# Optimization experiments

Measured on AMD Instinct MI355X. Metric: run time of the kernel, lower is better.

Reference implementation:

```python
import jax, jax.numpy as jnp
import numpy as np

B, S, D, F, H, E = 2, 1024, 1024, 4096, 16, 8
EPS = 1e-5


def _layernorm(x, w, b):
    m = jnp.mean(x, -1, keepdims=True)
    v = jnp.var(x, -1, keepdims=True)
    return (x - m) * jax.lax.rsqrt(v + EPS) * w + b


def _rope(x):
    # rotary embedding applied over full embed dim (split-half convention)
    b, s, d = x.shape
    half = d // 2
    inv = 1.0 / (10000.0 ** (jnp.arange(half, dtype=jnp.float32) / half))
    ang = jnp.arange(s, dtype=jnp.float32)[:, None] * inv[None, :]  # [S, half]
    cos, sin = jnp.cos(ang), jnp.sin(ang)
    x1, x2 = x[..., :half], x[..., half:]
    return jnp.concatenate([x1 * cos - x2 * sin, x1 * sin + x2 * cos], -1)


def setup_inputs() -> dict:
    key = jax.random.key(0)
    ks = jax.random.split(key, 9)
    sc = 0.02
    return {
        "x": jax.random.normal(ks[0], (B, S, D), jnp.float32),
        "ln1_w": jnp.ones((D,), jnp.float32),
        "ln1_b": jnp.zeros((D,), jnp.float32),
        "ln2_w": jnp.ones((D,), jnp.float32),
        "ln2_b": jnp.zeros((D,), jnp.float32),
        "w_qkv": jax.random.normal(ks[1], (3 * D, D), jnp.float32) * sc,
        "b_qkv": jnp.zeros((3 * D,), jnp.float32),
        "w_out": jax.random.normal(ks[2], (D, D), jnp.float32) * sc,
        "b_out": jnp.zeros((D,), jnp.float32),
        "w_router": jax.random.normal(ks[3], (D, E), jnp.float32) * sc,
        "wi": jax.random.normal(ks[4], (E, D, F), jnp.float32) * sc,  # per-expert wi (no bias)
        "wo": jax.random.normal(ks[5], (E, F // 2, D), jnp.float32) * sc,  # swiglu halves ffn dim
    }


def reference(x, ln1_w, ln1_b, ln2_w, ln2_b, w_qkv, b_qkv, w_out, b_out, w_router, wi, wo):
    # ---- pre-norm self-attention block ----
    residual = x
    h = _layernorm(x, ln1_w, ln1_b)
    h = _rope(h)
    qkv = h @ w_qkv.T + b_qkv  # [B,S,3D]
    q, k, v = jnp.split(qkv, 3, axis=-1)
    hd = D // H
    to_heads = lambda t: t.reshape(B, S, H, hd).transpose(0, 2, 1, 3)
    q, k, v = to_heads(q), to_heads(k), to_heads(v)
    scale = 1.0 / np.sqrt(hd).astype(np.float32)
    att = jax.nn.softmax(jnp.einsum('bhqd,bhkd->bhqk', q, k) * scale, axis=-1)
    o = jnp.einsum('bhqk,bhkd->bhqd', att, v).transpose(0, 2, 1, 3).reshape(B, S, D)
    o = o @ w_out.T + b_out
    x = residual + o  # attn dropout is identity at eval

    # ---- pre-norm sparse MoE FFN block ----
    residual = x
    h = _layernorm(x, ln2_w, ln2_b)
    # top-1 router in float32
    logits = h.astype(jnp.float32) @ w_router  # [B,S,E]
    probs = jax.nn.softmax(logits, axis=-1)
    mask = jax.nn.one_hot(jnp.argmax(probs, -1), E, dtype=h.dtype)  # expert_mask
    gate = probs.astype(h.dtype) * mask  # router_probs * expert_mask, [B,S,E]
    # dense all-expert compute, masked combine (same math as gather/scatter loop)
    hid = jnp.einsum('bsd,edf->bsef', h, wi)  # [B,S,E,F]
    a, g = jnp.split(hid, 2, axis=-1)
    act = jax.nn.silu(a) * g  # SwiGLU, [B,S,E,F/2]
    y = jnp.einsum('bsef,efd,bse->bsd', act, wo, gate)
    x = residual + y
    return x, logits
```

## Files before the change

### kernel.cpp

```cpp
#include <hip/hip_runtime.h>
#include <hip/hip_bf16.h>
#include <math.h>

#define BB 2
#define SS 1024
#define DD 1024
#define FF 4096
#define HH 16
#define EE 8
#define MM (BB*SS)
#define MAX_TILES 24

typedef __attribute__((ext_vector_type(8))) short bf16x8;
typedef __attribute__((ext_vector_type(8))) short s16x8;
typedef __attribute__((ext_vector_type(4))) float f32x4;

#define OFF_WIT  ((size_t)0)
#define OFF_WOT  ((size_t)67108864)
#define OFF_WQH  ((size_t)100663296)
#define OFF_WQL  ((size_t)106954752)
#define OFF_WOH  ((size_t)113246208)
#define OFF_WOL  ((size_t)115343360)
#define OFF_H1H  ((size_t)117440512)
#define OFF_H1L  ((size_t)121634816)
#define OFF_QKV  ((size_t)125829120)
#define OFF_OH   ((size_t)150994944)
#define OFF_OL   ((size_t)155189248)
#define OFF_X2   ((size_t)159383552)
#define OFF_H2B  ((size_t)167772160)
#define OFF_ACT  ((size_t)171966464)
#define OFF_GATE ((size_t)180879360)
#define OFF_EID  ((size_t)180887552)
#define OFF_PERM ((size_t)180895744)
#define OFF_CNT  ((size_t)180903936)
#define OFF_FILL ((size_t)180903968)
#define OFF_NT   ((size_t)180904000)
#define OFF_TE   ((size_t)180904192)
#define OFF_TS   ((size_t)180904320)
#define OFF_TR   ((size_t)180904448)
#define OFF_KSH  OFF_WQH
#define OFF_KSL  (OFF_WQH + 4194304)
#define OFF_VTH  OFF_H1H
#define OFF_VTL  OFF_H1L

__device__ __forceinline__ void gload16(const void* g, void* l) {
    __builtin_amdgcn_global_load_lds(
        (const __attribute__((address_space(1))) unsigned int*)g,
        (__attribute__((address_space(3))) unsigned int*)l, 16, 0, 0);
}

__device__ __forceinline__ short bfh(float v) {
    __hip_bfloat16 h = __float2bfloat16(v);
    return *(short*)&h;
}
__device__ __forceinline__ float bf2f(short s) {
    __hip_bfloat16 h = *(__hip_bfloat16*)&s;
    return __bfloat162float(h);
}

__device__ __forceinline__ void split_write(float v, __hip_bfloat16* hp, __hip_bfloat16* lp, size_t idx) {
    __hip_bfloat16 h = __float2bfloat16(v);
    hp[idx] = h;
    lp[idx] = __float2bfloat16(v - __bfloat162float(h));
}

__device__ __forceinline__ void tcvt64_body(const float* __restrict__ in, __hip_bfloat16* __restrict__ out,
                                            int R, int C, int r0, int c0, float* tile ) {
    int t = threadIdx.x;
    {
        int ri = t >> 2, cj = (t & 3) * 16;
        const float* ip = &in[(size_t)(r0 + ri) * C + c0 + cj];
#pragma unroll
        for (int k = 0; k < 4; ++k) {
            float4 v = *(const float4*)(ip + k * 4);
            tile[ri * 65 + cj + k * 4 + 0] = v.x;
            tile[ri * 65 + cj + k * 4 + 1] = v.y;
            tile[ri * 65 + cj + k * 4 + 2] = v.z;
            tile[ri * 65 + cj + k * 4 + 3] = v.w;
        }
    }
    __syncthreads();
    {
        int co = t >> 2, rj = (t & 3) * 16;
        bf16x8 v8a, v8b;
#pragma unroll
        for (int q = 0; q < 8; ++q) v8a[q] = bfh(tile[(rj + q) * 65 + co]);
#pragma unroll
        for (int q = 0; q < 8; ++q) v8b[q] = bfh(tile[(rj + 8 + q) * 65 + co]);
        __hip_bfloat16* op = &out[(size_t)(c0 + co) * R + r0 + rj];
        *(bf16x8*)op = v8a;
        *(bf16x8*)(op + 8) = v8b;
    }
}

__global__ void k_phase0(const float* __restrict__ x, const float* __restrict__ ln1w,
                         const float* __restrict__ ln1b,
                         __hip_bfloat16* __restrict__ h1H, __hip_bfloat16* __restrict__ h1L,
                         const float* __restrict__ w_qkv, __hip_bfloat16* __restrict__ wqH,
                         __hip_bfloat16* __restrict__ wqL) {
    __shared__ __align__(16) float smem[1032];
    int bid = blockIdx.x, t = threadIdx.x;
    if (bid < 2048) {
        int m = bid, s = m & (SS - 1);
        float* row = smem;
        float* red = smem + 1024;
        const float* xp = x + (size_t)m * DD;
        float sum = 0.f, sumsq = 0.f;
#pragma unroll
        for (int l = 0; l < 4; ++l) {
            int i = t + l * 256;
            float v = xp[i];
            row[i] = v;
            sum += v; sumsq += v * v;
        }
#pragma unroll
        for (int off = 32; off; off >>= 1) {
            sum   += __shfl_xor(sum, off);
            sumsq += __shfl_xor(sumsq, off);
        }
        int wid = t >> 6, lane = t & 63;
        if (lane == 0) { red[wid] = sum; red[4 + wid] = sumsq; }
        __syncthreads();
        sum   = red[0] + red[1] + red[2] + red[3];
        sumsq = red[4] + red[5] + red[6] + red[7];
        float mean = sum * (1.f / DD);
        float var  = sumsq * (1.f / DD) - mean * mean;
        float rstd = rsqrtf(var + 1e-5f);
        size_t base = (size_t)m * DD;
        const float kln = logf(10000.f) / 512.f;
#pragma unroll
        for (int l = 0; l < 2; ++l) {
            int i = t + l * 256;
            float n1 = (row[i]       - mean) * rstd * ln1w[i]       + ln1b[i];
            float n2 = (row[i + 512] - mean) * rstd * ln1w[i + 512] + ln1b[i + 512];
            float inv = expf(-(float)i * kln);
            float ang = (float)s * inv;
            float c = cosf(ang), sn = sinf(ang);
            split_write(n1 * c - n2 * sn,  h1H, h1L, base + i);
            split_write(n1 * sn + n2 * c, h1H, h1L, base + i + 512);
        }
    } else {
        int idx = (bid - 2048) * 256 + t;
        float4 v = ((const float4*)w_qkv)[idx];
        split_write(v.x, wqH, wqL, (size_t)idx * 4 + 0);
        split_write(v.y, wqH, wqL, (size_t)idx * 4 + 1);
        split_write(v.z, wqH, wqL, (size_t)idx * 4 + 2);
        split_write(v.w, wqH, wqL, (size_t)idx * 4 + 3);
    }
}

__global__ void k_qkv_mega(const __hip_bfloat16* __restrict__ Ah, const __hip_bfloat16* __restrict__ Al,
                           const __hip_bfloat16* __restrict__ Bh, const __hip_bfloat16* __restrict__ Bl,
                           const float* __restrict__ bias, float* __restrict__ Cf,
                           const float* __restrict__ wi, __hip_bfloat16* __restrict__ wiT,
                           const float* __restrict__ wo, __hip_bfloat16* __restrict__ woT,
                           const float* __restrict__ w_out, __hip_bfloat16* __restrict__ woH,
                           __hip_bfloat16* __restrict__ woL) {
    __shared__ __align__(16) char smem[32768];
    int bid = blockIdx.x;
    const int t = threadIdx.x;
    if (bid < 384) {
        const int N = 3072, K = DD;
        short* AsH = (short*)smem;
        short* AsL = (short*)(smem + 8192);
        short* BsH = (short*)(smem + 16384);
        short* BsL = (short*)(smem + 24576);
        int n0 = (bid % 24) * 128, m0 = (bid / 24) * 128;
        const int w = t >> 6, lane = t & 63;
        const int wr = w >> 1, wc = w & 1;
        const int sid = w * 64 + lane;

        f32x4 acc[4][4] = {};

        for (int k0 = 0; k0 < K; k0 += 32) {
#pragma unroll
            for (int j = 0; j < 2; ++j) {
                int id = j * 256 + sid;
                int rrow = id >> 2, sl = id & 3;
                int slog = sl ^ ((rrow >> 1) & 3);
                size_t lbase = (size_t)(j * 256 + w * 64) * 8;
                size_t gaoff = (size_t)(m0 + rrow) * K + k0 + slog * 8;
                gload16(Ah + gaoff, &AsH[lbase]);
                gload16(Al + gaoff, &AsL[lbase]);
                size_t gboff = (size_t)(n0 + rrow) * K + k0 + slog * 8;
                gload16(Bh + gboff, &BsH[lbase]);
                gload16(Bl + gboff, &BsL[lbase]);
            }
            __syncthreads();
            bf16x8 ah[4], al[4], bh[4], bl[4];
#pragma unroll
            for (int i = 0; i < 4; ++i) {
                int ra = wr * 64 + i * 16 + (lane & 15);
                int pa = (lane >> 4) ^ ((ra >> 1) & 3);
                ah[i] = *(const bf16x8*)&AsH[ra * 32 + pa * 8];
                al[i] = *(const bf16x8*)&AsL[ra * 32 + pa * 8];
                int rb = wc * 64 + i * 16 + (lane & 15);
                int pb = (lane >> 4) ^ ((rb >> 1) & 3);
                bh[i] = *(const bf16x8*)&BsH[rb * 32 + pb * 8];
                bl[i] = *(const bf16x8*)&BsL[rb * 32 + pb * 8];
            }
#pragma unroll
            for (int i = 0; i < 4; ++i)
#pragma unroll
                for (int n = 0; n < 4; ++n) {
                    acc[i][n] = __builtin_amdgcn_mfma_f32_16x16x32_bf16(ah[i], bh[n], acc[i][n], 0, 0, 0);
                    acc[i][n] = __builtin_amdgcn_mfma_f32_16x16x32_bf16(ah[i], bl[n], acc[i][n], 0, 0, 0);
                    acc[i][n] = __builtin_amdgcn_mfma_f32_16x16x32_bf16(al[i], bh[n], acc[i][n], 0, 0, 0);
                }
            __syncthreads();
        }

        int cn = n0 + wc * 64 + (lane & 15);
#pragma unroll
        for (int i = 0; i < 4; ++i) {
#pragma unroll
            for (int n = 0; n < 4; ++n) {
                int col = cn + n * 16;
#pragma unroll
                for (int q = 0; q < 4; ++q) {
                    int r = wr * 64 + i * 16 + (lane >> 4) * 4 + q;
                    Cf[(size_t)(m0 + r) * N + col] = acc[i][n][q] + bias[col];
                }
            }
        }
    } else if (bid < 8576) {
        int j = bid - 384;
        int e = j >> 10, rem = j & 1023;
        int ry = rem >> 6, cx = rem & 63;
        tcvt64_body(wi + (size_t)e * DD * FF, wiT + (size_t)e * DD * FF,
                    1024, 4096, ry * 64, cx * 64, (float*)smem);
    } else if (bid < 12672) {
        int j = bid - 8576;
        int e = j >> 9, rem = j & 511;
        int ry = rem >> 4, cx = rem & 15;
        tcvt64_body(wo + (size_t)e * 2048 * 1024, woT + (size_t)e * 2048 * 1024,
                    2048, 1024, ry * 64, cx * 64, (float*)smem);
    } else {
        int idx = (bid - 12672) * 256 + t;
        float4 v = ((const float4*)w_out)[idx];
        split_write(v.x, woH, woL, (size_t)idx * 4 + 0);
        split_write(v.y, woH, woL, (size_t)idx * 4 + 1);
        split_write(v.z, woH, woL, (size_t)idx * 4 + 2);
        split_write(v.w, woH, woL, (size_t)idx * 4 + 3);
    }
}

__global__ void k_mfma_split1(const __hip_bfloat16* __restrict__ Ah, const __hip_bfloat16* __restrict__ Al,
                              const __hip_bfloat16* __restrict__ Bh, const __hip_bfloat16* __restrict__ Bl,
                              const float* __restrict__ bias, const float* __restrict__ addsrc,
                              float* __restrict__ Cf, int M, int N, int K, int* __restrict__ zero17) {
    __shared__ __align__(16) short AsH[128 * 32];
    __shared__ __align__(16) short AsL[128 * 32];
    __shared__ __align__(16) short BsH[128 * 32];
    __shared__ __align__(16) short BsL[128 * 32];
    int m0 = blockIdx.y * 128, n0 = blockIdx.x * 128;
    const int t = threadIdx.x;
    if (blockIdx.x == 0 && blockIdx.y == 0 && t < 17) zero17[t] = 0;
    const int w = t >> 6, lane = t & 63;
    const int wr = w >> 1, wc = w & 1;
    const int sid = w * 64 + lane;

    f32x4 acc[4][4] = {};

    for (int k0 = 0; k0 < K; k0 += 32) {
#pragma unroll
        for (int j = 0; j < 2; ++j) {
            int id = j * 256 + sid;
            int rrow = id >> 2, sl = id & 3;
            int slog = sl ^ ((rrow >> 1) & 3);
            size_t lbase = (size_t)(j * 256 + w * 64) * 8;
            size_t gaoff = (size_t)(m0 + rrow) * K + k0 + slog * 8;
            gload16(Ah + gaoff, &AsH[lbase]);
            gload16(Al + gaoff, &AsL[lbase]);
            size_t gboff = (size_t)(n0 + rrow) * K + k0 + slog * 8;
            gload16(Bh + gboff, &BsH[lbase]);
            gload16(Bl + gboff, &BsL[lbase]);
        }
        __syncthreads();
        bf16x8 ah[4], al[4], bh[4], bl[4];
#pragma unroll
        for (int i = 0; i < 4; ++i) {
            int ra = wr * 64 + i * 16 + (lane & 15);
            int pa = (lane >> 4) ^ ((ra >> 1) & 3);
            ah[i] = *(const bf16x8*)&AsH[ra * 32 + pa * 8];
            al[i] = *(const bf16x8*)&AsL[ra * 32 + pa * 8];
            int rb = wc * 64 + i * 16 + (lane & 15);
            int pb = (lane >> 4) ^ ((rb >> 1) & 3);
            bh[i] = *(const bf16x8*)&BsH[rb * 32 + pb * 8];
            bl[i] = *(const bf16x8*)&BsL[rb * 32 + pb * 8];
        }
#pragma unroll
        for (int i = 0; i < 4; ++i)
#pragma unroll
            for (int n = 0; n < 4; ++n) {
                acc[i][n] = __builtin_amdgcn_mfma_f32_16x16x32_bf16(ah[i], bh[n], acc[i][n], 0, 0, 0);
                acc[i][n] = __builtin_amdgcn_mfma_f32_16x16x32_bf16(ah[i], bl[n], acc[i][n], 0, 0, 0);
                acc[i][n] = __builtin_amdgcn_mfma_f32_16x16x32_bf16(al[i], bh[n], acc[i][n], 0, 0, 0);
            }
        __syncthreads();
    }

    int cn = n0 + wc * 64 + (lane & 15);
#pragma unroll
    for (int i = 0; i < 4; ++i) {
#pragma unroll
        for (int n = 0; n < 4; ++n) {
            int col = cn + n * 16;
#pragma unroll
            for (int q = 0; q < 4; ++q) {
                int r = wr * 64 + i * 16 + (lane >> 4) * 4 + q;
                Cf[(size_t)(m0 + r) * N + col] =
                    acc[i][n][q] + bias[col] + addsrc[(size_t)(m0 + r) * N + col];
            }
        }
    }
}

__global__ void k_moe_up(const __hip_bfloat16* __restrict__ A,
                         const __hip_bfloat16* __restrict__ Bt,
                         __hip_bfloat16* __restrict__ act,
                         const int* __restrict__ perm,
                         const int* __restrict__ te, const int* __restrict__ ts,
                         const int* __restrict__ tr, const int* __restrict__ ntl) {
    __shared__ __align__(16) short As[128 * 32];
    __shared__ __align__(16) short Bs[128 * 32];
    __shared__ int permS[128];
    int tile = blockIdx.y;
    if (tile >= *ntl) return;
    int e = te[tile], rs = ts[tile], rows = tr[tile];
    if (threadIdx.x < 128) {
        int r = threadIdx.x;
        permS[r] = (r < rows) ? perm[rs + r] : 0;
    }
    __syncthreads();
    int c0 = blockIdx.x * 64;
    const int t = threadIdx.x;
    const int w = t >> 6, lane = t & 63;
    const int wr = w >> 1, wc = w & 1;
    const int sid = w * 64 + lane;
    const int g = lane >> 4, r16 = lane & 15;

    const __hip_bfloat16* Bp = Bt + (size_t)e * FF * DD;

    f32x4 acc[4][4] = {};

    for (int k0 = 0; k0 < DD; k0 += 32) {
#pragma unroll
        for (int j = 0; j < 2; ++j) {
            int id = j * 256 + sid;
            int rrow = id >> 2, sl = id & 3;
            int slog = sl ^ ((rrow >> 1) & 3);
            size_t lbase = (size_t)(j * 256 + w * 64) * 8;
            gload16(A + (size_t)permS[rrow] * DD + k0 + slog * 8, &As[lbase]);
            int q = rrow >> 4, rr = rrow & 15;
            int wrow = c0 + (q >> 2) * 32 + ((q & 3) >> 1) * 16 + rr + (q & 1) * 2048;
            gload16(Bp + (size_t)wrow * DD + k0 + slog * 8, &Bs[lbase]);
        }
        __syncthreads();
        bf16x8 af[4], bfr[4];
#pragma unroll
        for (int i = 0; i < 4; ++i) {
            int ra = wr * 64 + i * 16 + r16;
            int pa = g ^ ((ra >> 1) & 3);
            af[i] = *(const bf16x8*)&As[ra * 32 + pa * 8];
            int rb = wc * 64 + i * 16 + r16;
            int pb = g ^ ((rb >> 1) & 3);
            bfr[i] = *(const bf16x8*)&Bs[rb * 32 + pb * 8];
        }
#pragma unroll
        for (int i = 0; i < 4; ++i)
#pragma unroll
            for (int n = 0; n < 4; ++n)
                acc[i][n] = __builtin_amdgcn_mfma_f32_16x16x32_bf16(af[i], bfr[n], acc[i][n], 0, 0, 0);
        __syncthreads();
    }

#pragma unroll
    for (int i = 0; i < 4; ++i) {
#pragma unroll
        for (int p2 = 0; p2 < 2; ++p2) {
            int col = c0 + wc * 32 + p2 * 16 + r16;
#pragma unroll
            for (int q = 0; q < 4; ++q) {
                int r = wr * 64 + i * 16 + g * 4 + q;
                if (r < rows) {
                    float a  = acc[i][2 * p2][q];
                    float gv = acc[i][2 * p2 + 1][q];
                    act[(size_t)(rs + r) * 2048 + col] =
                        __float2bfloat16((a / (1.f + expf(-a))) * gv);
                }
            }
        }
    }
}

__global__ void k_moe_dn(const __hip_bfloat16* __restrict__ A,
                         const __hip_bfloat16* __restrict__ Bt,
                         const float* __restrict__ addsrc, float* __restrict__ Cf,
                         const int* __restrict__ perm,
                         const int* __restrict__ te, const int* __restrict__ ts,
                         const int* __restrict__ tr, const int* __restrict__ ntl,
                         const float* __restrict__ gate) {
    __shared__ __align__(16) short As[128 * 32];
    __shared__ __align__(16) short Bs[128 * 32];
    __shared__ int permS[128];
    int tile = blockIdx.y;
    if (tile >= *ntl) return;
    int e = te[tile], rs = ts[tile], rows = tr[tile];
    if (threadIdx.x < 128) {
        int r = threadIdx.x;
        permS[r] = (r < rows) ? perm[rs + r] : 0;
    }
    __syncthreads();
    int n0 = blockIdx.x * 128;
    const int t = threadIdx.x;
    const int w = t >> 6, lane = t & 63;
    const int wr = w >> 1, wc = w & 1;
    const int sid = w * 64 + lane;
    const int K = FF / 2;

    const __hip_bfloat16* Bp = Bt + (size_t)e * DD * (FF / 2);

    f32x4 acc[4][4] = {};

    for (int k0 = 0; k0 < K; k0 += 32) {
#pragma unroll
        for (int j = 0; j < 2; ++j) {
            int id = j * 256 + sid;
            int rrow = id >> 2, sl = id & 3;
            int slog = sl ^ ((rrow >> 1) & 3);
            size_t lbase = (size_t)(j * 256 + w * 64) * 8;
            gload16(A + (size_t)(rs + rrow) * K + k0 + slog * 8, &As[lbase]);
            gload16(Bp + (size_t)(n0 + rrow) * K + k0 + slog * 8, &Bs[lbase]);
        }
        __syncthreads();
        bf16x8 af[4], bfr[4];
#pragma unroll
        for (int i = 0; i < 4; ++i) {
            int ra = wr * 64 + i * 16 + (lane & 15);
            int pa = (lane >> 4) ^ ((ra >> 1) & 3);
            af[i] = *(const bf16x8*)&As[ra * 32 + pa * 8];
            int rb = wc * 64 + i * 16 + (lane & 15);
            int pb = (lane >> 4) ^ ((rb >> 1) & 3);
            bfr[i] = *(const bf16x8*)&Bs[rb * 32 + pb * 8];
        }
#pragma unroll
        for (int i = 0; i < 4; ++i)
#pragma unroll
            for (int n = 0; n < 4; ++n)
                acc[i][n] = __builtin_amdgcn_mfma_f32_16x16x32_bf16(af[i], bfr[n], acc[i][n], 0, 0, 0);
        __syncthreads();
    }

    int cn = n0 + wc * 64 + (lane & 15);
#pragma unroll
    for (int i = 0; i < 4; ++i) {
#pragma unroll
        for (int n = 0; n < 4; ++n) {
            int col = cn + n * 16;
#pragma unroll
            for (int q = 0; q < 4; ++q) {
                int r = wr * 64 + i * 16 + (lane >> 4) * 4 + q;
                if (r >= rows) continue;
                int tok = permS[r];
                Cf[(size_t)tok * DD + col] = addsrc[(size_t)tok * DD + col] + gate[tok] * acc[i][n][q];
            }
        }
    }
}

__global__ void k_prep(const float* __restrict__ qkv, short* __restrict__ KH, short* __restrict__ KL,
                       short* __restrict__ VH, short* __restrict__ VL) {
    __shared__ float tile[64][65];
    int b = blockIdx.z, h = blockIdx.y, s0 = blockIdx.x * 64;
    int t = threadIdx.x;
    int row = t >> 2, c0 = (t & 3) * 16;
    const float* kp = qkv + (size_t)(b * SS + s0 + row) * 3072 + 1024 + h * 64 + c0;
    const float* vp = kp + 1024;
    {
        size_t krow = ((size_t)(b * HH + h) * SS + s0 + row) * 64;
        int key = (s0 + row) & 7;
#pragma unroll
        for (int g2 = 0; g2 < 2; ++g2) {
            s16x8 hv, lv;
#pragma unroll
            for (int j = 0; j < 8; ++j) {
                float v = kp[g2 * 8 + j];
                short hh = bfh(v);
                hv[j] = hh; lv[j] = bfh(v - bf2f(hh));
            }
            int p = ((c0 >> 3) + g2) ^ key;
            *(s16x8*)&KH[krow + p * 8] = hv;
            *(s16x8*)&KL[krow + p * 8] = lv;
        }
    }
#pragma unroll
    for (int j = 0; j < 16; ++j) tile[row][c0 + j] = vp[j];
    __syncthreads();
    {
        int d = t >> 2, sc = (t & 3) * 16;
        size_t vrow = ((size_t)(b * HH + h) * 64 + d) * SS + s0;
        int key = d & 7;
#pragma unroll
        for (int g2 = 0; g2 < 2; ++g2) {
            s16x8 hv, lv;
#pragma unroll
            for (int j = 0; j < 8; ++j) {
                float v = tile[sc + g2 * 8 + j][d];
                short hh = bfh(v);
                hv[j] = hh; lv[j] = bfh(v - bf2f(hh));
            }
            int p = ((sc >> 3) + g2) ^ key;
            *(s16x8*)&VH[vrow + p * 8] = hv;
            *(s16x8*)&VL[vrow + p * 8] = lv;
        }
    }
}

#define LDP 72
__global__ __launch_bounds__(512, 1)
void k_attn_mfma(const float* __restrict__ qkv,
                 const short* __restrict__ KH, const short* __restrict__ KL,
                 const short* __restrict__ VH, const short* __restrict__ VL,
                 __hip_bfloat16* __restrict__ ohi, __hip_bfloat16* __restrict__ olo) {
    __shared__ __align__(16) short Ks[2][64 * 64], Kl2[2][64 * 64], Vs[2][64 * 64], Vl2[2][64 * 64];
    __shared__ __align__(16) short PhS[8][16 * LDP], PlS[8][16 * LDP];
    int id = blockIdx.x;
    int xcd = id & 7, slot = id >> 3;
    int bh = xcd * 4 + (slot >> 3);
    int q0 = (slot & 7) * 128;
    int b = bh >> 4, h = bh & 15;
    int t = threadIdx.x;
    int w = t >> 6, lane = t & 63;
    int g = lane >> 4, r16 = lane & 15;
    int srow = t >> 3, sslot = t & 7;

    const size_t kbase = ((size_t)bh * SS) * 64;
    const size_t vbase = ((size_t)bh * 64) * SS;

    bf16x8 qfh[2], qfl[2];
    {
        const float* qp = qkv + (size_t)(b * SS + q0 + w * 16 + r16) * 3072 + h * 64;
#pragma unroll
        for (int ks = 0; ks < 2; ++ks) {
            float vv[8];
            *(float4*)&vv[0] = *(const float4*)(qp + ks * 32 + g * 8);
            *(float4*)&vv[4] = *(const float4*)(qp + ks * 32 + g * 8 + 4);
#pragma unroll
            for (int j = 0; j < 8; ++j) {
                float sv = vv[j] * 0.125f;
                short hh = bfh(sv);
                qfh[ks][j] = hh;
                qfl[ks][j] = bfh(sv - bf2f(hh));
            }
        }
    }

    float mrun[4], lrun[4];
    f32x4 oacc[4] = {};
#pragma unroll
    for (int q = 0; q < 4; ++q) { mrun[q] = -1e30f; lrun[q] = 0.f; }

    gload16(KH + kbase + (size_t)srow * 64 + sslot * 8, &Ks[0][w * 512]);
    gload16(KL + kbase + (size_t)srow * 64 + sslot * 8, &Kl2[0][w * 512]);
    gload16(VH + vbase + (size_t)srow * SS + sslot * 8, &Vs[0][w * 512]);
    gload16(VL + vbase + (size_t)srow * SS + sslot * 8, &Vl2[0][w * 512]);
    __syncthreads();

    int cur = 0;
    for (int k0 = 0; k0 < SS; k0 += 64) {
        if (k0 + 64 < SS) {
            int kn = k0 + 64;
            gload16(KH + kbase + (size_t)(kn + srow) * 64 + sslot * 8, &Ks[cur ^ 1][w * 512]);
            gload16(KL + kbase + (size_t)(kn + srow) * 64 + sslot * 8, &Kl2[cur ^ 1][w * 512]);
            gload16(VH + vbase + (size_t)srow * SS + kn + sslot * 8,   &Vs[cur ^ 1][w * 512]);
            gload16(VL + vbase + (size_t)srow * SS + kn + sslot * 8,   &Vl2[cur ^ 1][w * 512]);
        }

        f32x4 accs[4] = {};
#pragma unroll
        for (int ks = 0; ks < 2; ++ks) {
            bf16x8 kfh[4], kfl[4];
#pragma unroll
            for (int n = 0; n < 4; ++n) {
                int rb = n * 16 + r16;
                int p = (ks * 4 + g) ^ (r16 & 7);
                kfh[n] = *(const bf16x8*)&Ks[cur][rb * 64 + p * 8];
                kfl[n] = *(const bf16x8*)&Kl2[cur][rb * 64 + p * 8];
            }
            __builtin_amdgcn_s_setprio(1);
#pragma unroll
            for (int n = 0; n < 4; ++n) {
                accs[n] = __builtin_amdgcn_mfma_f32_16x16x32_bf16(qfh[ks], kfh[n], accs[n], 0, 0, 0);
                accs[n] = __builtin_amdgcn_mfma_f32_16x16x32_bf16(qfh[ks], kfl[n], accs[n], 0, 0, 0);
                accs[n] = __builtin_amdgcn_mfma_f32_16x16x32_bf16(qfl[ks], kfh[n], accs[n], 0, 0, 0);
            }
            __builtin_amdgcn_s_setprio(0);
        }

        float mn[4], corr[4], psum[4];
#pragma unroll
        for (int q = 0; q < 4; ++q) {
            float m = fmaxf(fmaxf(accs[0][q], accs[1][q]), fmaxf(accs[2][q], accs[3][q]));
            m = fmaxf(m, __shfl_xor(m, 1));
            m = fmaxf(m, __shfl_xor(m, 2));
            m = fmaxf(m, __shfl_xor(m, 4));
            m = fmaxf(m, __shfl_xor(m, 8));
            mn[q] = fmaxf(mrun[q], m);
            corr[q] = expf(mrun[q] - mn[q]);
            mrun[q] = mn[q];
            psum[q] = 0.f;
        }
#pragma unroll
        for (int n = 0; n < 4; ++n)
#pragma unroll
            for (int q = 0; q < 4; ++q) {
                float p = expf(accs[n][q] - mn[q]);
                psum[q] += p;
                short ph = bfh(p);
                PhS[w][(g * 4 + q) * LDP + n * 16 + r16] = ph;
                PlS[w][(g * 4 + q) * LDP + n * 16 + r16] = bfh(p - bf2f(ph));
            }
#pragma unroll
        for (int q = 0; q < 4; ++q) {
            psum[q] += __shfl_xor(psum[q], 1);
            psum[q] += __shfl_xor(psum[q], 2);
            psum[q] += __shfl_xor(psum[q], 4);
            psum[q] += __shfl_xor(psum[q], 8);
            lrun[q] = lrun[q] * corr[q] + psum[q];
#pragma unroll
            for (int n = 0; n < 4; ++n) oacc[n][q] *= corr[q];
        }

#pragma unroll
        for (int ks = 0; ks < 2; ++ks) {
            bf16x8 vfh[4], vfl[4];
#pragma unroll
            for (int n = 0; n < 4; ++n) {
                int rb = n * 16 + r16;
                int p = (ks * 4 + g) ^ (r16 & 7);
                vfh[n] = *(const bf16x8*)&Vs[cur][rb * 64 + p * 8];
                vfl[n] = *(const bf16x8*)&Vl2[cur][rb * 64 + p * 8];
            }
            bf16x8 pfh = *(const bf16x8*)&PhS[w][r16 * LDP + ks * 32 + g * 8];
            bf16x8 pfl = *(const bf16x8*)&PlS[w][r16 * LDP + ks * 32 + g * 8];
            __builtin_amdgcn_s_setprio(1);
#pragma unroll
            for (int n = 0; n < 4; ++n) {
                oacc[n] = __builtin_amdgcn_mfma_f32_16x16x32_bf16(pfh, vfh[n], oacc[n], 0, 0, 0);
                oacc[n] = __builtin_amdgcn_mfma_f32_16x16x32_bf16(pfh, vfl[n], oacc[n], 0, 0, 0);
                oacc[n] = __builtin_amdgcn_mfma_f32_16x16x32_bf16(pfl, vfh[n], oacc[n], 0, 0, 0);
            }
            __builtin_amdgcn_s_setprio(0);
        }
        __syncthreads();
        cur ^= 1;
    }

    float invl[4];
#pragma unroll
    for (int q = 0; q < 4; ++q) invl[q] = 1.f / lrun[q];
#pragma unroll
    for (int n = 0; n < 4; ++n) {
        int col = h * 64 + n * 16 + r16;
#pragma unroll
        for (int q = 0; q < 4; ++q) {
            int rowg = b * SS + q0 + w * 16 + g * 4 + q;
            split_write(oacc[n][q] * invl[q], ohi, olo, (size_t)rowg * DD + col);
        }
    }
}

__global__ void k_ln2_router(const float* __restrict__ x2, const float* __restrict__ w,
                             const float* __restrict__ b, const float* __restrict__ wr,
                             __hip_bfloat16* __restrict__ h2b, float* __restrict__ logits,
                             float* __restrict__ gate, int* __restrict__ eid,
                             int* __restrict__ counts) {
    int m = blockIdx.x, t = threadIdx.x;
    __shared__ float red[8];
    __shared__ float racc[4][8];
    const float* xp = x2 + (size_t)m * DD;
    float v[4];
    float sum = 0.f, sumsq = 0.f;
#pragma unroll
    for (int l = 0; l < 4; ++l) {
        v[l] = xp[t + l * 256];
        sum += v[l]; sumsq += v[l] * v[l];
    }
#pragma unroll
    for (int off = 32; off; off >>= 1) {
        sum   += __shfl_xor(sum, off);
        sumsq += __shfl_xor(sumsq, off);
    }
    int wid = t >> 6, lane = t & 63;
    if (lane == 0) { red[wid] = sum; red[4 + wid] = sumsq; }
    __syncthreads();
    sum   = red[0] + red[1] + red[2] + red[3];
    sumsq = red[4] + red[5] + red[6] + red[7];
    float mean = sum * (1.f / DD);
    float var  = sumsq * (1.f / DD) - mean * mean;
    float rstd = rsqrtf(var + 1e-5f);
    float acc[EE] = {};
#pragma unroll
    for (int l = 0; l < 4; ++l) {
        int i = t + l * 256;
        float hv = (v[l] - mean) * rstd * w[i] + b[i];
        h2b[(size_t)m * DD + i] = __float2bfloat16(hv);
        const float* wp = wr + (size_t)i * EE;
#pragma unroll
        for (int n = 0; n < EE; ++n) acc[n] += hv * wp[n];
    }
#pragma unroll
    for (int off = 32; off; off >>= 1)
#pragma unroll
        for (int n = 0; n < EE; ++n) acc[n] += __shfl_xor(acc[n], off);
    if (lane == 0)
#pragma unroll
        for (int n = 0; n < EE; ++n) racc[wid][n] = acc[n];
    __syncthreads();
    if (t == 0) {
        float lg[EE];
#pragma unroll
        for (int n = 0; n < EE; ++n) lg[n] = racc[0][n] + racc[1][n] + racc[2][n] + racc[3][n];
        float mx = lg[0]; int best = 0;
#pragma unroll
        for (int n = 1; n < EE; ++n) if (lg[n] > mx) { mx = lg[n]; best = n; }
        float den = 0.f;
#pragma unroll
        for (int n = 0; n < EE; ++n) den += expf(lg[n] - mx);
        gate[m] = 1.f / den;
        eid[m] = best;
        atomicAdd(&counts[best], 1);
#pragma unroll
        for (int n = 0; n < EE; ++n) logits[(size_t)m * EE + n] = lg[n];
    }
}

__global__ void k_offscatter(const int* __restrict__ counts,
                             int* __restrict__ te, int* __restrict__ ts, int* __restrict__ tr,
                             int* __restrict__ ntl, const int* __restrict__ eid,
                             int* __restrict__ fill, int* __restrict__ perm) {
    __shared__ int soffs[EE];
    int t = threadIdx.x;
    if (t == 0) {
        int off = 0, nt = 0;
        for (int e = 0; e < EE; ++e) {
            soffs[e] = off;
            int c = counts[e];
            for (int t0 = 0; t0 < c; t0 += 128) {
                te[nt] = e; ts[nt] = off + t0; tr[nt] = (c - t0 < 128) ? (c - t0) : 128; ++nt;
            }
            off += c;
        }
        *ntl = nt;
    }
    __syncthreads();
#pragma unroll
    for (int tok = t; tok < MM; tok += 1024) {
        int e = eid[tok];
        int pos = soffs[e] + atomicAdd(&fill[e], 1);
        perm[pos] = tok;
    }
}

extern "C" void kernel_launch(void* const* d_in, const int* in_sizes, int n_in,
                              void* d_out, int out_size, void* d_ws, size_t ws_size,
                              hipStream_t stream) {
    const float* x     = (const float*)d_in[0];
    const float* ln1w  = (const float*)d_in[1];
    const float* ln1b  = (const float*)d_in[2];
    const float* ln2w  = (const float*)d_in[3];
    const float* ln2b  = (const float*)d_in[4];
    const float* w_qkv = (const float*)d_in[5];
    const float* b_qkv = (const float*)d_in[6];
    const float* w_out = (const float*)d_in[7];
    const float* b_out = (const float*)d_in[8];
    const float* w_rtr = (const float*)d_in[9];
    const float* wi    = (const float*)d_in[10];
    const float* wo    = (const float*)d_in[11];
    float* out = (float*)d_out;

    char* wsb = (char*)d_ws;
    __hip_bfloat16* wiT  = (__hip_bfloat16*)(wsb + OFF_WIT);
    __hip_bfloat16* woT  = (__hip_bfloat16*)(wsb + OFF_WOT);
    __hip_bfloat16* wqH  = (__hip_bfloat16*)(wsb + OFF_WQH);
    __hip_bfloat16* wqL  = (__hip_bfloat16*)(wsb + OFF_WQL);
    __hip_bfloat16* woH  = (__hip_bfloat16*)(wsb + OFF_WOH);
    __hip_bfloat16* woL  = (__hip_bfloat16*)(wsb + OFF_WOL);
    __hip_bfloat16* h1H  = (__hip_bfloat16*)(wsb + OFF_H1H);
    __hip_bfloat16* h1L  = (__hip_bfloat16*)(wsb + OFF_H1L);
    float*          qkvF = (float*)(wsb + OFF_QKV);
    __hip_bfloat16* oH   = (__hip_bfloat16*)(wsb + OFF_OH);
    __hip_bfloat16* oL   = (__hip_bfloat16*)(wsb + OFF_OL);
    float*          x2F  = (float*)(wsb + OFF_X2);
    __hip_bfloat16* h2B  = (__hip_bfloat16*)(wsb + OFF_H2B);
    __hip_bfloat16* actB = (__hip_bfloat16*)(wsb + OFF_ACT);
    short* KSH = (short*)(wsb + OFF_KSH);
    short* KSL = (short*)(wsb + OFF_KSL);
    short* VTH = (short*)(wsb + OFF_VTH);
    short* VTL = (short*)(wsb + OFF_VTL);
    float* gate = (float*)(wsb + OFF_GATE);
    int* eid    = (int*)(wsb + OFF_EID);
    int* perm   = (int*)(wsb + OFF_PERM);
    int* counts = (int*)(wsb + OFF_CNT);
    int* fill   = (int*)(wsb + OFF_FILL);
    int* ntl    = (int*)(wsb + OFF_NT);
    int* te     = (int*)(wsb + OFF_TE);
    int* tsx    = (int*)(wsb + OFF_TS);
    int* trx    = (int*)(wsb + OFF_TR);

    k_phase0<<<5120, 256, 0, stream>>>(x, ln1w, ln1b, h1H, h1L, w_qkv, wqH, wqL);
    k_qkv_mega<<<13696, 256, 0, stream>>>(h1H, h1L, wqH, wqL, b_qkv, qkvF,
                                          wi, wiT, wo, woT, w_out, woH, woL);
    k_prep<<<dim3(SS / 64, HH, BB), 256, 0, stream>>>(qkvF, KSH, KSL, VTH, VTL);
    k_attn_mfma<<<256, 512, 0, stream>>>(qkvF, KSH, KSL, VTH, VTL, oH, oL);
    k_mfma_split1<<<dim3(DD / 128, MM / 128), 256, 0, stream>>>(
        oH, oL, woH, woL, b_out, x, x2F, MM, DD, DD, counts);
    k_ln2_router<<<MM, 256, 0, stream>>>(x2F, ln2w, ln2b, w_rtr, h2B,
                                         out + (size_t)MM * DD, gate, eid, counts);
    k_offscatter<<<1, 1024, 0, stream>>>(counts, te, tsx, trx, ntl, eid, fill, perm);
    k_moe_up<<<dim3(2048 / 64, MAX_TILES), 256, 0, stream>>>(
        h2B, wiT, actB, perm, te, tsx, trx, ntl);
    k_moe_dn<<<dim3(DD / 128, MAX_TILES), 256, 0, stream>>>(
        actB, woT, x2F, out, perm, te, tsx, trx, ntl, gate);
}
```

Measured before the change: 334.9 us.

## Use 64-row tiles for out-proj and MoE down, overlap wo transpose with MoE up

The attention output projection and the MoE down-projection now use 64x128 tiles instead of 128x128, so each launches more blocks and the tail is less ragged. Offscatter builds a second tile list at 64-row granularity for the down-projection. The wo transpose/convert moves out of the QKV mega-kernel and runs as extra blocks appended to the MoE up launch, so it fills idle CUs there. Smaller tiles reread weights more often, and the up kernel's grid grows, which may delay the down kernel's dependency.

```diff
diff --git a/kernel.cpp b/kernel.cpp
--- a/kernel.cpp
+++ b/kernel.cpp
@@ -10,6 +10,7 @@
 #define EE 8
 #define MM (BB*SS)
 #define MAX_TILES 24
+#define MAX_TILES2 40
 
 typedef __attribute__((ext_vector_type(8))) short bf16x8;
 typedef __attribute__((ext_vector_type(8))) short s16x8;
@@ -38,6 +39,10 @@
 #define OFF_TE   ((size_t)180904192)
 #define OFF_TS   ((size_t)180904320)
 #define OFF_TR   ((size_t)180904448)
+#define OFF_TE2  ((size_t)180904576)
+#define OFF_TS2  ((size_t)180904768)
+#define OFF_TR2  ((size_t)180904960)
+#define OFF_NT2  ((size_t)180905152)
 #define OFF_KSH  OFF_WQH
 #define OFF_KSL  (OFF_WQH + 4194304)
 #define OFF_VTH  OFF_H1H
@@ -153,7 +158,6 @@
                            const __hip_bfloat16* __restrict__ Bh, const __hip_bfloat16* __restrict__ Bl,
                            const float* __restrict__ bias, float* __restrict__ Cf,
                            const float* __restrict__ wi, __hip_bfloat16* __restrict__ wiT,
-                           const float* __restrict__ wo, __hip_bfloat16* __restrict__ woT,
                            const float* __restrict__ w_out, __hip_bfloat16* __restrict__ woH,
                            __hip_bfloat16* __restrict__ woL) {
     __shared__ __align__(16) char smem[32768];
@@ -229,14 +233,8 @@
         int ry = rem >> 6, cx = rem & 63;
         tcvt64_body(wi + (size_t)e * DD * FF, wiT + (size_t)e * DD * FF,
                     1024, 4096, ry * 64, cx * 64, (float*)smem);
-    } else if (bid < 12672) {
-        int j = bid - 8576;
-        int e = j >> 9, rem = j & 511;
-        int ry = rem >> 4, cx = rem & 15;
-        tcvt64_body(wo + (size_t)e * 2048 * 1024, woT + (size_t)e * 2048 * 1024,
-                    2048, 1024, ry * 64, cx * 64, (float*)smem);
     } else {
-        int idx = (bid - 12672) * 256 + t;
+        int idx = (bid - 8576) * 256 + t;
         float4 v = ((const float4*)w_out)[idx];
         split_write(v.x, woH, woL, (size_t)idx * 4 + 0);
         split_write(v.y, woH, woL, (size_t)idx * 4 + 1);
@@ -245,54 +243,64 @@
     }
 }
 
-__global__ void k_mfma_split1(const __hip_bfloat16* __restrict__ Ah, const __hip_bfloat16* __restrict__ Al,
-                              const __hip_bfloat16* __restrict__ Bh, const __hip_bfloat16* __restrict__ Bl,
-                              const float* __restrict__ bias, const float* __restrict__ addsrc,
-                              float* __restrict__ Cf, int M, int N, int K, int* __restrict__ zero17) {
-    __shared__ __align__(16) short AsH[128 * 32];
-    __shared__ __align__(16) short AsL[128 * 32];
+__global__ void k_oproj64(const __hip_bfloat16* __restrict__ Ah, const __hip_bfloat16* __restrict__ Al,
+                          const __hip_bfloat16* __restrict__ Bh, const __hip_bfloat16* __restrict__ Bl,
+                          const float* __restrict__ bias, const float* __restrict__ addsrc,
+                          float* __restrict__ Cf, int* __restrict__ zero17) {
+    __shared__ __align__(16) short AsH[64 * 32];
+    __shared__ __align__(16) short AsL[64 * 32];
     __shared__ __align__(16) short BsH[128 * 32];
     __shared__ __align__(16) short BsL[128 * 32];
-    int m0 = blockIdx.y * 128, n0 = blockIdx.x * 128;
+    const int N = DD, K = DD;
+    int bid = blockIdx.x;
+    int m0 = (bid >> 3) * 64, n0 = (bid & 7) * 128;
     const int t = threadIdx.x;
-    if (blockIdx.x == 0 && blockIdx.y == 0 && t < 17) zero17[t] = 0;
+    if (bid == 0 && t < 17) zero17[t] = 0;
     const int w = t >> 6, lane = t & 63;
-    const int wr = w >> 1, wc = w & 1;
     const int sid = w * 64 + lane;
-
-    f32x4 acc[4][4] = {};
+    const int g = lane >> 4, r16 = lane & 15;
+
+    f32x4 acc[4][2] = {};
 
     for (int k0 = 0; k0 < K; k0 += 32) {
+        {
+            int rrow = sid >> 2, sl = sid & 3;
+            int slog = sl ^ ((rrow >> 1) & 3);
+            size_t lbase = (size_t)(w * 64) * 8;
+            size_t gaoff = (size_t)(m0 + rrow) * K + k0 + slog * 8;
+            gload16(Ah + gaoff, &AsH[lbase]);
+            gload16(Al + gaoff, &AsL[lbase]);
+        }
 #pragma unroll
         for (int j = 0; j < 2; ++j) {
             int id = j * 256 + sid;
             int rrow = id >> 2, sl = id & 3;
             int slog = sl ^ ((rrow >> 1) & 3);
             size_t lbase = (size_t)(j * 256 + w * 64) * 8;
-            size_t gaoff = (size_t)(m0 + rrow) * K + k0 + slog * 8;
-            gload16(Ah + gaoff, &AsH[lbase]);
-            gload16(Al + gaoff, &AsL[lbase]);
             size_t gboff = (size_t)(n0 + rrow) * K + k0 + slog * 8;
             gload16(Bh + gboff, &BsH[lbase]);
             gload16(Bl + gboff, &BsL[lbase]);
         }
         __syncthreads();
-        bf16x8 ah[4], al[4], bh[4], bl[4];
+        bf16x8 ah[4], al[4], bh[2], bl[2];
 #pragma unroll
         for (int i = 0; i < 4; ++i) {
-            int ra = wr * 64 + i * 16 + (lane & 15);
-            int pa = (lane >> 4) ^ ((ra >> 1) & 3);
+            int ra = i * 16 + r16;
+            int pa = g ^ ((ra >> 1) & 3);
             ah[i] = *(const bf16x8*)&AsH[ra * 32 + pa * 8];
             al[i] = *(const bf16x8*)&AsL[ra * 32 + pa * 8];
-            int rb = wc * 64 + i * 16 + (lane & 15);
-            int pb = (lane >> 4) ^ ((rb >> 1) & 3);
-            bh[i] = *(const bf16x8*)&BsH[rb * 32 + pb * 8];
-            bl[i] = *(const bf16x8*)&BsL[rb * 32 + pb * 8];
+        }
+#pragma unroll
+        for (int n = 0; n < 2; ++n) {
+            int rb = w * 32 + n * 16 + r16;
+            int pb = g ^ ((rb >> 1) & 3);
+            bh[n] = *(const bf16x8*)&BsH[rb * 32 + pb * 8];
+            bl[n] = *(const bf16x8*)&BsL[rb * 32 + pb * 8];
         }
 #pragma unroll
         for (int i = 0; i < 4; ++i)
 #pragma unroll
-            for (int n = 0; n < 4; ++n) {
+            for (int n = 0; n < 2; ++n) {
                 acc[i][n] = __builtin_amdgcn_mfma_f32_16x16x32_bf16(ah[i], bh[n], acc[i][n], 0, 0, 0);
                 acc[i][n] = __builtin_amdgcn_mfma_f32_16x16x32_bf16(ah[i], bl[n], acc[i][n], 0, 0, 0);
                 acc[i][n] = __builtin_amdgcn_mfma_f32_16x16x32_bf16(al[i], bh[n], acc[i][n], 0, 0, 0);
@@ -300,17 +308,16 @@
         __syncthreads();
     }
 
-    int cn = n0 + wc * 64 + (lane & 15);
 #pragma unroll
     for (int i = 0; i < 4; ++i) {
 #pragma unroll
-        for (int n = 0; n < 4; ++n) {
-            int col = cn + n * 16;
+        for (int n = 0; n < 2; ++n) {
+            int col = n0 + w * 32 + n * 16 + r16;
 #pragma unroll
             for (int q = 0; q < 4; ++q) {
-                int r = wr * 64 + i * 16 + (lane >> 4) * 4 + q;
-                Cf[(size_t)(m0 + r) * N + col] =
-                    acc[i][n][q] + bias[col] + addsrc[(size_t)(m0 + r) * N + col];
+                int r = m0 + i * 16 + g * 4 + q;
+                Cf[(size_t)r * N + col] =
+                    acc[i][n][q] + bias[col] + addsrc[(size_t)r * N + col];
             }
         }
     }
@@ -321,20 +328,28 @@
                          __hip_bfloat16* __restrict__ act,
                          const int* __restrict__ perm,
                          const int* __restrict__ te, const int* __restrict__ ts,
-                         const int* __restrict__ tr, const int* __restrict__ ntl) {
-    __shared__ __align__(16) short As[128 * 32];
-    __shared__ __align__(16) short Bs[128 * 32];
-    __shared__ int permS[128];
-    int tile = blockIdx.y;
+                         const int* __restrict__ tr, const int* __restrict__ ntl,
+                         const float* __restrict__ wo, __hip_bfloat16* __restrict__ woT) {
+    __shared__ __align__(16) char smem[17408];
+    int bid = blockIdx.x;
+    const int t = threadIdx.x;
+    if (bid >= 768) {
+        int j = bid - 768;
+        int e = j >> 9, rem = j & 511;
+        int ry = rem >> 4, cx = rem & 15;
+        tcvt64_body(wo + (size_t)e * 2048 * 1024, woT + (size_t)e * 2048 * 1024,
+                    2048, 1024, ry * 64, cx * 64, (float*)smem);
+        return;
+    }
+    short* As = (short*)smem;
+    short* Bs = (short*)(smem + 8192);
+    int* permS = (int*)(smem + 16384);
+    int tile = bid / 32;
     if (tile >= *ntl) return;
     int e = te[tile], rs = ts[tile], rows = tr[tile];
-    if (threadIdx.x < 128) {
-        int r = threadIdx.x;
-        permS[r] = (r < rows) ? perm[rs + r] : 0;
-    }
+    if (t < 128) permS[t] = (t < rows) ? perm[rs + t] : 0;
     __syncthreads();
-    int c0 = blockIdx.x * 64;
-    const int t = threadIdx.x;
+    int c0 = (bid & 31) * 64;
     const int w = t >> 6, lane = t & 63;
     const int wr = w >> 1, wc = w & 1;
     const int sid = w * 64 + lane;
@@ -398,69 +413,73 @@
                          const __hip_bfloat16* __restrict__ Bt,
                          const float* __restrict__ addsrc, float* __restrict__ Cf,
                          const int* __restrict__ perm,
-                         const int* __restrict__ te, const int* __restrict__ ts,
-                         const int* __restrict__ tr, const int* __restrict__ ntl,
+                         const int* __restrict__ te2, const int* __restrict__ ts2,
+                         const int* __restrict__ tr2, const int* __restrict__ ntl2,
                          const float* __restrict__ gate) {
-    __shared__ __align__(16) short As[128 * 32];
+    __shared__ __align__(16) short As[64 * 32];
     __shared__ __align__(16) short Bs[128 * 32];
-    __shared__ int permS[128];
+    __shared__ int permS[64];
     int tile = blockIdx.y;
-    if (tile >= *ntl) return;
-    int e = te[tile], rs = ts[tile], rows = tr[tile];
-    if (threadIdx.x < 128) {
-        int r = threadIdx.x;
-        permS[r] = (r < rows) ? perm[rs + r] : 0;
-    }
+    if (tile >= *ntl2) return;
+    int e = te2[tile], rs = ts2[tile], rows = tr2[tile];
+    const int t = threadIdx.x;
+    if (t < 64) permS[t] = (t < rows) ? perm[rs + t] : 0;
     __syncthreads();
     int n0 = blockIdx.x * 128;
-    const int t = threadIdx.x;
     const int w = t >> 6, lane = t & 63;
-    const int wr = w >> 1, wc = w & 1;
     const int sid = w * 64 + lane;
+    const int g = lane >> 4, r16 = lane & 15;
     const int K = FF / 2;
 
     const __hip_bfloat16* Bp = Bt + (size_t)e * DD * (FF / 2);
 
-    f32x4 acc[4][4] = {};
+    f32x4 acc[4][2] = {};
 
     for (int k0 = 0; k0 < K; k0 += 32) {
+        {
+            int rrow = sid >> 2, sl = sid & 3;
+            int slog = sl ^ ((rrow >> 1) & 3);
+            size_t lbase = (size_t)(w * 64) * 8;
+            gload16(A + (size_t)(rs + rrow) * K + k0 + slog * 8, &As[lbase]);
+        }
 #pragma unroll
         for (int j = 0; j < 2; ++j) {
             int id = j * 256 + sid;
             int rrow = id >> 2, sl = id & 3;
             int slog = sl ^ ((rrow >> 1) & 3);
             size_t lbase = (size_t)(j * 256 + w * 64) * 8;
-            gload16(A + (size_t)(rs + rrow) * K + k0 + slog * 8, &As[lbase]);
             gload16(Bp + (size_t)(n0 + rrow) * K + k0 + slog * 8, &Bs[lbase]);
         }
         __syncthreads();
-        bf16x8 af[4], bfr[4];
+        bf16x8 af[4], bfr[2];
 #pragma unroll
         for (int i = 0; i < 4; ++i) {
-            int ra = wr * 64 + i * 16 + (lane & 15);
-            int pa = (lane >> 4) ^ ((ra >> 1) & 3);
+            int ra = i * 16 + r16;
+            int pa = g ^ ((ra >> 1) & 3);
             af[i] = *(const bf16x8*)&As[ra * 32 + pa * 8];
-            int rb = wc * 64 + i * 16 + (lane & 15);
-            int pb = (lane >> 4) ^ ((rb >> 1) & 3);
-            bfr[i] = *(const bf16x8*)&Bs[rb * 32 + pb * 8];
+        }
+#pragma unroll
+        for (int n = 0; n < 2; ++n) {
+            int rb = w * 32 + n * 16 + r16;
+            int pb = g ^ ((rb >> 1) & 3);
+            bfr[n] = *(const bf16x8*)&Bs[rb * 32 + pb * 8];
         }
 #pragma unroll
         for (int i = 0; i < 4; ++i)
 #pragma unroll
-            for (int n = 0; n < 4; ++n)
+            for (int n = 0; n < 2; ++n)
                 acc[i][n] = __builtin_amdgcn_mfma_f32_16x16x32_bf16(af[i], bfr[n], acc[i][n], 0, 0, 0);
         __syncthreads();
     }
 
-    int cn = n0 + wc * 64 + (lane & 15);
 #pragma unroll
     for (int i = 0; i < 4; ++i) {
 #pragma unroll
-        for (int n = 0; n < 4; ++n) {
-            int col = cn + n * 16;
+        for (int n = 0; n < 2; ++n) {
+            int col = n0 + w * 32 + n * 16 + r16;
 #pragma unroll
             for (int q = 0; q < 4; ++q) {
-                int r = wr * 64 + i * 16 + (lane >> 4) * 4 + q;
+                int r = i * 16 + g * 4 + q;
                 if (r >= rows) continue;
                 int tok = permS[r];
                 Cf[(size_t)tok * DD + col] = addsrc[(size_t)tok * DD + col] + gate[tok] * acc[i][n][q];
@@ -738,21 +757,28 @@
 
 __global__ void k_offscatter(const int* __restrict__ counts,
                              int* __restrict__ te, int* __restrict__ ts, int* __restrict__ tr,
-                             int* __restrict__ ntl, const int* __restrict__ eid,
+                             int* __restrict__ ntl,
+                             int* __restrict__ te2, int* __restrict__ ts2, int* __restrict__ tr2,
+                             int* __restrict__ ntl2,
+                             const int* __restrict__ eid,
                              int* __restrict__ fill, int* __restrict__ perm) {
     __shared__ int soffs[EE];
     int t = threadIdx.x;
     if (t == 0) {
-        int off = 0, nt = 0;
+        int off = 0, nt = 0, nt2 = 0;
         for (int e = 0; e < EE; ++e) {
             soffs[e] = off;
             int c = counts[e];
             for (int t0 = 0; t0 < c; t0 += 128) {
                 te[nt] = e; ts[nt] = off + t0; tr[nt] = (c - t0 < 128) ? (c - t0) : 128; ++nt;
             }
+            for (int t0 = 0; t0 < c; t0 += 64) {
+                te2[nt2] = e; ts2[nt2] = off + t0; tr2[nt2] = (c - t0 < 64) ? (c - t0) : 64; ++nt2;
+            }
             off += c;
         }
         *ntl = nt;
+        *ntl2 = nt2;
     }
     __syncthreads();
 #pragma unroll
@@ -808,19 +834,23 @@
     int* te     = (int*)(wsb + OFF_TE);
     int* tsx    = (int*)(wsb + OFF_TS);
     int* trx    = (int*)(wsb + OFF_TR);
+    int* te2    = (int*)(wsb + OFF_TE2);
+    int* ts2    = (int*)(wsb + OFF_TS2);
+    int* tr2    = (int*)(wsb + OFF_TR2);
+    int* ntl2   = (int*)(wsb + OFF_NT2);
 
     k_phase0<<<5120, 256, 0, stream>>>(x, ln1w, ln1b, h1H, h1L, w_qkv, wqH, wqL);
-    k_qkv_mega<<<13696, 256, 0, stream>>>(h1H, h1L, wqH, wqL, b_qkv, qkvF,
-                                          wi, wiT, wo, woT, w_out, woH, woL);
+    k_qkv_mega<<<9600, 256, 0, stream>>>(h1H, h1L, wqH, wqL, b_qkv, qkvF,
+                                         wi, wiT, w_out, woH, woL);
     k_prep<<<dim3(SS / 64, HH, BB), 256, 0, stream>>>(qkvF, KSH, KSL, VTH, VTL);
     k_attn_mfma<<<256, 512, 0, stream>>>(qkvF, KSH, KSL, VTH, VTL, oH, oL);
-    k_mfma_split1<<<dim3(DD / 128, MM / 128), 256, 0, stream>>>(
-        oH, oL, woH, woL, b_out, x, x2F, MM, DD, DD, counts);
+    k_oproj64<<<256, 256, 0, stream>>>(oH, oL, woH, woL, b_out, x, x2F, counts);
     k_ln2_router<<<MM, 256, 0, stream>>>(x2F, ln2w, ln2b, w_rtr, h2B,
                                          out + (size_t)MM * DD, gate, eid, counts);
-    k_offscatter<<<1, 1024, 0, stream>>>(counts, te, tsx, trx, ntl, eid, fill, perm);
-    k_moe_up<<<dim3(2048 / 64, MAX_TILES), 256, 0, stream>>>(
-        h2B, wiT, actB, perm, te, tsx, trx, ntl);
-    k_moe_dn<<<dim3(DD / 128, MAX_TILES), 256, 0, stream>>>(
-        actB, woT, x2F, out, perm, te, tsx, trx, ntl, gate);
-}
+    k_offscatter<<<1, 1024, 0, stream>>>(counts, te, tsx, trx, ntl,
+                                         te2, ts2, tr2, ntl2, eid, fill, perm);
+    k_moe_up<<<768 + 4096, 256, 0, stream>>>(h2B, wiT, actB, perm, te, tsx, trx, ntl,
+                                             wo, woT);
+    k_moe_dn<<<dim3(DD / 128, MAX_TILES2), 256, 0, stream>>>(
+        actB, woT, x2F, out, perm, te2, ts2, tr2, ntl2, gate);
+}
```

Measured after the change: 316.4 us. 1.06x faster.
